# Kernel optimization log

Hardware: AMD Instinct MI355X
Metric: run time of the kernel (lower is better)

The kernel has to match this reference:

```python
import jax, jax.numpy as jnp
import numpy as np

NUM_STAB = 1e-3  # numerical_stabilizer for relu kernel


def _relu_feature(x, proj):
    # x: [B, L, H, D], proj: [M, D] -> [B, L, H, M]
    ratio = 1.0 / jnp.sqrt(jnp.asarray(proj.shape[0], x.dtype))
    return jax.nn.relu(ratio * jnp.einsum('blhd,md->blhm', x, proj)) + NUM_STAB


def setup_inputs() -> dict:
    key = jax.random.key(0)
    k1, k2, k3, k4, k5 = jax.random.split(key, 5)
    B, L, H, D, M = 16, 576, 12, 64, 8  # L = length_of_side**2 = 24**2
    return {
        'query': jax.random.normal(k1, (B, L, H, D), dtype=jnp.float32),
        'key': jax.random.normal(k2, (B, L, H, D), dtype=jnp.float32),
        'value': jax.random.normal(k3, (B, L, H, D), dtype=jnp.float32),
        'projection_matrix': jax.random.normal(k4, (M, D), dtype=jnp.float32),
        # RPE mask is nonnegative per-head mixing matrix [H, L, L]
        'mask_matrix': jax.random.uniform(k5, (H, L, L), dtype=jnp.float32),
    }


def reference(query, key, value, projection_matrix, mask_matrix):
    # ReLU kernel features (projection_matrix_type='relu')
    q_prime = _relu_feature(query, projection_matrix)  # [B, L, H, M]
    k_prime = _relu_feature(key, projection_matrix)    # [B, L, H, M]
    B, L, H, M = k_prime.shape
    D = value.shape[-1]

    # D_1[b,l,h,m,d] = k'[b,l,h,m] * v[b,l,h,d], flattened over (m,d)
    D_1 = jnp.einsum('blhm,blhd->blhmd', k_prime, value).reshape(B, L, H, M * D)
    # mask-matrix causal/RPE mixing over the L dimension (per head)
    D_1_hat = jnp.einsum('hij,bjhc->bihc', mask_matrix, D_1).reshape(B, L, H, M, D)
    D_2_hat = jnp.einsum('hij,bjhm->bihm', mask_matrix, k_prime)  # [B, L, H, M]

    av_attention = jnp.einsum('blhm,blhmd->blhd', q_prime, D_1_hat)  # [B, L, H, D]
    ks_sum = jnp.sum(D_2_hat, axis=1)                                # [B, H, M]
    normalizer = jnp.einsum('blhm,bhm->blh', q_prime, ks_sum)        # [B, L, H]
    return av_attention / normalizer[..., None]
```

## Files before the change

kernel.cpp:

```cpp
#include <hip/hip_runtime.h>
#include <hip/hip_bf16.h>


#define B_ 16
#define L_ 576
#define H_ 12
#define D_ 64
#define M_ 8
#define NUM_STAB 1e-3f
#define RATIO 0.35355339059327373f

typedef __attribute__((ext_vector_type(8))) short short8;
typedef __attribute__((ext_vector_type(4))) float f32x4;

union Pack {
    uint4 u4;
    short8 s8;
    uint2 u2[2];
    unsigned u[4];
    unsigned short us[8];
};

__device__ inline unsigned short f2bf(float x) {
    union { float f; unsigned u; } a; a.f = x;
    unsigned r = (a.u + 0x7FFFu + ((a.u >> 16) & 1u)) >> 16;
    return (unsigned short)r;
}
__device__ inline unsigned pk2(float lo, float hi) {
    __hip_bfloat162 h = __float22bfloat162_rn(make_float2(lo, hi));
    union { __hip_bfloat162 b; unsigned u; } c; c.b = h;
    return c.u;
}

#define WS_QP_OFF (H_ * L_)
#define QP_ELEMS  ((size_t)B_ * H_ * L_ * M_)

__global__ __launch_bounds__(256) void feat_kernel(const float* __restrict__ q,
                                                   const float* __restrict__ k,
                                                   const float* __restrict__ proj,
                                                   const float* __restrict__ mask,
                                                   unsigned short* __restrict__ qp,
                                                   unsigned short* __restrict__ kp,
                                                   float* __restrict__ cmask) {
    __shared__ float cred[4][16];
    const int lc = blockIdx.x, h = blockIdx.y, b = blockIdx.z, t = threadIdx.x;
    const int wv = t >> 6, l = t & 63, r8 = l >> 3, c8 = l & 7;
    const int row = lc * 32 + wv * 8 + r8;

    float4 pj0[8], pj1[8];
#pragma unroll
    for (int m = 0; m < 8; ++m) {
        pj0[m] = *(const float4*)(proj + m * 64 + c8 * 8);
        pj1[m] = *(const float4*)(proj + m * 64 + c8 * 8 + 4);
    }

#pragma unroll
    for (int s = 0; s < 2; ++s) {
        const float* src = s ? k : q;
        unsigned short* dst = s ? kp : qp;
        const float* xp = src + (((size_t)b * L_ + row) * H_ + h) * D_ + c8 * 8;
        float4 x0 = *(const float4*)xp;
        float4 x1 = *(const float4*)(xp + 4);
        x0.x *= RATIO; x0.y *= RATIO; x0.z *= RATIO; x0.w *= RATIO;
        x1.x *= RATIO; x1.y *= RATIO; x1.z *= RATIO; x1.w *= RATIO;
        float p[8];
#pragma unroll
        for (int m = 0; m < 8; ++m) {
            p[m] = x0.x * pj0[m].x + x0.y * pj0[m].y + x0.z * pj0[m].z + x0.w * pj0[m].w
                 + x1.x * pj1[m].x + x1.y * pj1[m].y + x1.z * pj1[m].z + x1.w * pj1[m].w;
        }
#pragma unroll
        for (int st = 1; st <= 4; st <<= 1) {
#pragma unroll
            for (int m = 0; m < 8; ++m) p[m] += __shfl_xor(p[m], st, 64);
        }
        float r = p[0];
        r = (c8 == 1) ? p[1] : r;
        r = (c8 == 2) ? p[2] : r;
        r = (c8 == 3) ? p[3] : r;
        r = (c8 == 4) ? p[4] : r;
        r = (c8 == 5) ? p[5] : r;
        r = (c8 == 6) ? p[6] : r;
        r = (c8 == 7) ? p[7] : r;
        r = fmaxf(r, 0.f) + NUM_STAB;
        dst[((size_t)(b * H_ + h) * L_ + row) * 8 + c8] = f2bf(r);
    }

    if (b < 2) {
        const int c = t & 15, rg = t >> 4;
        const int col0 = lc * 32 + b * 16;
        const float* mb = mask + (size_t)h * L_ * L_ + col0 + c;
        float a = 0.f;
#pragma unroll 4
        for (int k2 = 0; k2 < 36; ++k2) a += mb[(size_t)(rg + 16 * k2) * L_];
        a += __shfl_xor(a, 16, 64);
        a += __shfl_xor(a, 32, 64);
        if ((l >> 4) == 0) cred[wv][c] = a;
        __syncthreads();
        if (t < 16) cmask[h * L_ + col0 + t] = cred[0][t] + cred[1][t] + cred[2][t] + cred[3][t];
    }
}

__global__ __launch_bounds__(256, 4) void attn_kernel(const float* __restrict__ v,
                                                      const float* __restrict__ mask,
                                                      const unsigned short* __restrict__ qp,
                                                      const unsigned short* __restrict__ kp,
                                                      const float* __restrict__ cmask,
                                                      float* __restrict__ out) {
    __shared__ __align__(16) unsigned short Sp[4 * 16 * 72];
    __shared__ __align__(16) unsigned short Bt[2][64 * 72];
    __shared__ float cms[576];

    const int t = threadIdx.x;
    int id = blockIdx.x;
    const int bhi = id & 7; id >>= 3;
    const int blo = id & 1; id >>= 1;
    const int it = id % 9, h = id / 9;
    const int b = bhi * 2 + blo;
    const int i0 = it * 64;

    const int wv = t >> 6, l = t & 63, c15 = l & 15, kq = l >> 4;

    {
        const float* cmg = cmask + h * L_;
#pragma unroll
        for (int rep = 0; rep < 3; ++rep) {
            int idx = t + rep * 256;
            if (idx < 576) {
                int p = idx / 36, rem = idx - p * 36;
                int jt9 = rem >> 2, kqi = rem & 3;
                int j = jt9 * 64 + ((p >> 2) << 4) + 4 * kqi + (p & 3);
                cms[idx] = cmg[j];
            }
        }
    }

    const float* maskbase = mask + (size_t)h * L_ * L_ + (size_t)(i0 + 16 * wv + c15) * L_;
    const unsigned short* kpb = kp + (size_t)(b * H_ + h) * L_ * 8;
    const float* vb = v + ((size_t)b * L_ * H_ + h) * D_ + l;

    short8 Bq;
    {
        Pack pk; pk.u4 = make_uint4(0, 0, 0, 0);
        if (kq == 0) {
            const unsigned short* qpb = qp + ((size_t)(b * H_ + h) * L_ + i0 + 16 * wv + c15) * 8;
            pk.u4 = *(const uint4*)qpb;
        }
        Bq = pk.s8;
    }

    unsigned short* SpW = Sp + wv * 16 * 72;

    f32x4 acc0 = {0.f, 0.f, 0.f, 0.f}, acc1 = acc0, acc2 = acc0, acc3 = acc0;
    float nacc = 0.f;

    float vf[16];
    float4 mv[4];
    uint4 kraw0 = make_uint4(0, 0, 0, 0), kraw1 = kraw0;
    {
#pragma unroll
        for (int qv = 0; qv < 16; ++qv) vf[qv] = vb[(size_t)(16 * wv + qv) * (H_ * D_)];
#pragma unroll
        for (int T = 0; T < 4; ++T) mv[T] = *(const float4*)(maskbase + 16 * T + 4 * kq);
        if (kq < 2) {
            kraw0 = *(const uint4*)(kpb + (size_t)(16 * kq + c15) * 8);
            kraw1 = *(const uint4*)(kpb + (size_t)(32 + 16 * kq + c15) * 8);
        }
    }

    __syncthreads();

    for (int jt = 0; jt < 9; ++jt) {
        const int j0 = jt * 64;
        const int slab = jt & 1;

        f32x4 s[4];
        const f32x4 zz = {0.f, 0.f, 0.f, 0.f};
#pragma unroll
        for (int hh = 0; hh < 2; ++hh) {
            uint4 kr = hh ? kraw1 : kraw0;
            Pack a0, a1;
            a1.u[0] = __shfl_down(kr.x, 16, 64);
            a1.u[1] = __shfl_down(kr.y, 16, 64);
            a1.u[2] = __shfl_down(kr.z, 16, 64);
            a1.u[3] = __shfl_down(kr.w, 16, 64);
            if (kq == 0) {
                a0.u4 = kr;
            } else {
                a0.u4 = make_uint4(0, 0, 0, 0);
                a1.u4 = make_uint4(0, 0, 0, 0);
            }
            s[2 * hh]     = __builtin_amdgcn_mfma_f32_16x16x32_bf16(a0.s8, Bq, zz, 0, 0, 0);
            s[2 * hh + 1] = __builtin_amdgcn_mfma_f32_16x16x32_bf16(a1.s8, Bq, zz, 0, 0, 0);
        }

        {
            Pack p0, p1;
#pragma unroll
            for (int qv = 0; qv < 4; ++qv) p0.u[qv] = pk2(vf[2 * qv], vf[2 * qv + 1]);
#pragma unroll
            for (int qv = 0; qv < 4; ++qv) p1.u[qv] = pk2(vf[8 + 2 * qv], vf[9 + 2 * qv]);
            *(uint4*)&Bt[slab][l * 72 + 16 * wv] = p0.u4;
            *(uint4*)&Bt[slab][l * 72 + 16 * wv + 8] = p1.u4;
        }

#pragma unroll
        for (int T = 0; T < 4; ++T) {
            const float* cp = &cms[(T * 4) * 36 + jt * 4 + kq];
            float c0 = cp[0], c1 = cp[36], c2 = cp[72], c3 = cp[108];
            nacc += c0 * s[T][0] + c1 * s[T][1] + c2 * s[T][2] + c3 * s[T][3];
            float4 m4 = mv[T];
            uint2 st2;
            st2.x = pk2(s[T][0] * m4.x, s[T][1] * m4.y);
            st2.y = pk2(s[T][2] * m4.z, s[T][3] * m4.w);
            *(uint2*)&SpW[c15 * 72 + 16 * T + 4 * kq] = st2;
        }

        {
            const int jn = (jt < 8) ? j0 + 64 : 0;
#pragma unroll
            for (int qv = 0; qv < 16; ++qv) vf[qv] = vb[(size_t)(jn + 16 * wv + qv) * (H_ * D_)];
#pragma unroll
            for (int T = 0; T < 4; ++T) mv[T] = *(const float4*)(maskbase + jn + 16 * T + 4 * kq);
            if (kq < 2) {
                kraw0 = *(const uint4*)(kpb + (size_t)(jn + 16 * kq + c15) * 8);
                kraw1 = *(const uint4*)(kpb + (size_t)(jn + 32 + 16 * kq + c15) * 8);
            }
        }

        __syncthreads();

        {
            short8 As0 = *(const short8*)&SpW[c15 * 72 + kq * 8];
            short8 As1 = *(const short8*)&SpW[c15 * 72 + 32 + kq * 8];
#pragma unroll
            for (int di = 0; di < 4; ++di) {
                const unsigned short* bp = &Bt[slab][(16 * di + c15) * 72 + kq * 8];
                short8 B0 = *(const short8*)bp;
                short8 B1 = *(const short8*)(bp + 32);
                f32x4* ap = (di == 0) ? &acc0 : (di == 1) ? &acc1 : (di == 2) ? &acc2 : &acc3;
                *ap = __builtin_amdgcn_mfma_f32_16x16x32_bf16(As0, B0, *ap, 0, 0, 0);
                *ap = __builtin_amdgcn_mfma_f32_16x16x32_bf16(As1, B1, *ap, 0, 0, 0);
            }
        }
    }

    nacc += __shfl_xor(nacc, 16, 64);
    nacc += __shfl_xor(nacc, 32, 64);
    float iv[4];
#pragma unroll
    for (int r = 0; r < 4; ++r) iv[r] = 1.0f / __shfl(nacc, 4 * kq + r, 64);

    float* ob = out + (((size_t)b * L_ + i0 + 16 * wv + 4 * kq) * H_ + h) * D_ + c15;
    const f32x4 aa[4] = {acc0, acc1, acc2, acc3};
#pragma unroll
    for (int di = 0; di < 4; ++di)
#pragma unroll
        for (int r = 0; r < 4; ++r)
            ob[(size_t)r * (H_ * D_) + 16 * di] = aa[di][r] * iv[r];
}

extern "C" void kernel_launch(void* const* d_in, const int* in_sizes, int n_in,
                              void* d_out, int out_size, void* d_ws, size_t ws_size,
                              hipStream_t stream) {
    const float* q    = (const float*)d_in[0];
    const float* k    = (const float*)d_in[1];
    const float* v    = (const float*)d_in[2];
    const float* proj = (const float*)d_in[3];
    const float* mask = (const float*)d_in[4];
    float* out = (float*)d_out;

    float* ws = (float*)d_ws;
    float* cmask = ws;
    unsigned short* qp_w = (unsigned short*)(ws + WS_QP_OFF);
    unsigned short* kp_w = qp_w + QP_ELEMS;

    feat_kernel<<<dim3(L_ / 32, H_, B_), 256, 0, stream>>>(q, k, proj, mask, qp_w, kp_w, cmask);
    attn_kernel<<<1728, 256, 0, stream>>>(v, mask, qp_w, kp_w, cmask, out);
}
```

Measured before the change: 182.8 us.

## Pre-transpose V to bf16 in feature kernel and precompute normalizer weights

The feature kernel now also converts V to bf16 in a per-tile transposed layout, so the attention kernel loads it with wide vector loads instead of strided scalar float loads and per-iteration packing. The normalizer is refactored algebraically: a new small kernel computes the mask-column-sum-weighted sum of k' per (b,h), and the attention kernel computes the normalizer with a single dot product at the end instead of accumulating it every tile. The QK MFMA loading is simplified, the launch bound is raised to 5 blocks per CU, and the per-block shared column-mask staging is dropped. In exchange there is an extra kernel launch plus extra workspace traffic for the transposed V.

```diff
diff --git a/kernel.cpp b/kernel.cpp
--- a/kernel.cpp
+++ b/kernel.cpp
@@ -31,17 +31,23 @@
     union { __hip_bfloat162 b; unsigned u; } c; c.b = h;
     return c.u;
 }
-
-#define WS_QP_OFF (H_ * L_)
+__device__ inline float bf2f(unsigned short u) {
+    union { unsigned u; float f; } c; c.u = (unsigned)u << 16; return c.f;
+}
+
+#define WS_W_OFF  (H_ * L_)
+#define WS_QP_OFF (H_ * L_ + B_ * H_ * M_)
 #define QP_ELEMS  ((size_t)B_ * H_ * L_ * M_)
 
 __global__ __launch_bounds__(256) void feat_kernel(const float* __restrict__ q,
                                                    const float* __restrict__ k,
+                                                   const float* __restrict__ v,
                                                    const float* __restrict__ proj,
                                                    const float* __restrict__ mask,
                                                    unsigned short* __restrict__ qp,
                                                    unsigned short* __restrict__ kp,
-                                                   float* __restrict__ cmask) {
+                                                   float* __restrict__ cmask,
+                                                   unsigned short* __restrict__ vt) {
     __shared__ float cred[4][16];
     const int lc = blockIdx.x, h = blockIdx.y, b = blockIdx.z, t = threadIdx.x;
     const int wv = t >> 6, l = t & 63, r8 = l >> 3, c8 = l & 7;
@@ -84,6 +90,20 @@
         r = (c8 == 7) ? p[7] : r;
         r = fmaxf(r, 0.f) + NUM_STAB;
         dst[((size_t)(b * H_ + h) * L_ + row) * 8 + c8] = f2bf(r);
+    }
+
+    {
+        const int dv = t >> 2;
+        const int jl = (lc & 1) * 32 + (t & 3) * 8;
+        const int jt9 = lc >> 1;
+        const float* vsrc = v + (((size_t)b * L_ + jt9 * 64 + jl) * H_ + h) * D_ + dv;
+        float tv[8];
+#pragma unroll
+        for (int e = 0; e < 8; ++e) tv[e] = vsrc[(size_t)e * (H_ * D_)];
+        Pack pv;
+#pragma unroll
+        for (int q4 = 0; q4 < 4; ++q4) pv.u[q4] = pk2(tv[2 * q4], tv[2 * q4 + 1]);
+        *(uint4*)&vt[((size_t)(b * H_ + h) * 9 + jt9) * 4096 + dv * 64 + jl] = pv.u4;
     }
 
     if (b < 2) {
@@ -101,15 +121,44 @@
     }
 }
 
-__global__ __launch_bounds__(256, 4) void attn_kernel(const float* __restrict__ v,
-                                                      const float* __restrict__ mask,
+__global__ __launch_bounds__(64) void wsum_kernel(const unsigned short* __restrict__ kp,
+                                                  const float* __restrict__ cmask,
+                                                  float* __restrict__ wbuf) {
+    const int bh = blockIdx.x, lx = threadIdx.x;
+    const int h = bh % H_;
+    const unsigned short* kpb = kp + (size_t)bh * L_ * 8;
+    const float* cm = cmask + h * L_;
+    float a[8] = {0.f, 0.f, 0.f, 0.f, 0.f, 0.f, 0.f, 0.f};
+    for (int j = lx; j < L_; j += 64) {
+        const float c = cm[j];
+        Pack pk; pk.u4 = *(const uint4*)(kpb + (size_t)j * 8);
+#pragma unroll
+        for (int m = 0; m < 8; ++m) a[m] += c * bf2f(pk.us[m]);
+    }
+#pragma unroll
+    for (int st = 1; st < 64; st <<= 1) {
+#pragma unroll
+        for (int m = 0; m < 8; ++m) a[m] += __shfl_xor(a[m], st, 64);
+    }
+    float r = a[0];
+    r = (lx == 1) ? a[1] : r;
+    r = (lx == 2) ? a[2] : r;
+    r = (lx == 3) ? a[3] : r;
+    r = (lx == 4) ? a[4] : r;
+    r = (lx == 5) ? a[5] : r;
+    r = (lx == 6) ? a[6] : r;
+    r = (lx == 7) ? a[7] : r;
+    if (lx < 8) wbuf[(size_t)bh * 8 + lx] = r;
+}
+
+__global__ __launch_bounds__(256, 5) void attn_kernel(const float* __restrict__ mask,
                                                       const unsigned short* __restrict__ qp,
                                                       const unsigned short* __restrict__ kp,
-                                                      const float* __restrict__ cmask,
+                                                      const unsigned short* __restrict__ vt,
+                                                      const float* __restrict__ wbuf,
                                                       float* __restrict__ out) {
     __shared__ __align__(16) unsigned short Sp[4 * 16 * 72];
     __shared__ __align__(16) unsigned short Bt[2][64 * 72];
-    __shared__ float cms[576];
 
     const int t = threadIdx.x;
     int id = blockIdx.x;
@@ -120,136 +169,122 @@
     const int i0 = it * 64;
 
     const int wv = t >> 6, l = t & 63, c15 = l & 15, kq = l >> 4;
-
-    {
-        const float* cmg = cmask + h * L_;
-#pragma unroll
-        for (int rep = 0; rep < 3; ++rep) {
-            int idx = t + rep * 256;
-            if (idx < 576) {
-                int p = idx / 36, rem = idx - p * 36;
-                int jt9 = rem >> 2, kqi = rem & 3;
-                int j = jt9 * 64 + ((p >> 2) << 4) + 4 * kqi + (p & 3);
-                cms[idx] = cmg[j];
-            }
-        }
-    }
+    const int bd = t >> 3, bg = t & 7;
+    const int vt_off = bd * 64 + bg * 8;
 
     const float* maskbase = mask + (size_t)h * L_ * L_ + (size_t)(i0 + 16 * wv + c15) * L_;
     const unsigned short* kpb = kp + (size_t)(b * H_ + h) * L_ * 8;
-    const float* vb = v + ((size_t)b * L_ * H_ + h) * D_ + l;
+    const unsigned short* vtb = vt + (size_t)(b * H_ + h) * 9 * 4096;
+    unsigned short* SpW = Sp + wv * 16 * 72;
 
     short8 Bq;
     {
         Pack pk; pk.u4 = make_uint4(0, 0, 0, 0);
-        if (kq == 0) {
-            const unsigned short* qpb = qp + ((size_t)(b * H_ + h) * L_ + i0 + 16 * wv + c15) * 8;
-            pk.u4 = *(const uint4*)qpb;
-        }
+        if (kq == 0)
+            pk.u4 = *(const uint4*)(qp + ((size_t)(b * H_ + h) * L_ + i0 + 16 * wv + c15) * 8);
         Bq = pk.s8;
     }
 
-    unsigned short* SpW = Sp + wv * 16 * 72;
-
     f32x4 acc0 = {0.f, 0.f, 0.f, 0.f}, acc1 = acc0, acc2 = acc0, acc3 = acc0;
-    float nacc = 0.f;
-
-    float vf[16];
-    float4 mv[4];
-    uint4 kraw0 = make_uint4(0, 0, 0, 0), kraw1 = kraw0;
-    {
-#pragma unroll
-        for (int qv = 0; qv < 16; ++qv) vf[qv] = vb[(size_t)(16 * wv + qv) * (H_ * D_)];
-#pragma unroll
-        for (int T = 0; T < 4; ++T) mv[T] = *(const float4*)(maskbase + 16 * T + 4 * kq);
-        if (kq < 2) {
-            kraw0 = *(const uint4*)(kpb + (size_t)(16 * kq + c15) * 8);
-            kraw1 = *(const uint4*)(kpb + (size_t)(32 + 16 * kq + c15) * 8);
-        }
-    }
-
-    __syncthreads();
+    const f32x4 zz = {0.f, 0.f, 0.f, 0.f};
+
+    uint4 a0 = make_uint4(0, 0, 0, 0), a1 = a0, a2 = a0, a3 = a0;
+    uint4 vt0, vt1;
+    float4 mv0, mv1, mv2, mv3;
+    if (kq == 0) {
+        a0 = *(const uint4*)(kpb + (size_t)(c15) * 8);
+        a1 = *(const uint4*)(kpb + (size_t)(16 + c15) * 8);
+        a2 = *(const uint4*)(kpb + (size_t)(32 + c15) * 8);
+        a3 = *(const uint4*)(kpb + (size_t)(48 + c15) * 8);
+    }
+    vt0 = *(const uint4*)(vtb + vt_off);
+    vt1 = *(const uint4*)(vtb + 2048 + vt_off);
+    mv0 = *(const float4*)(maskbase + 0 + 4 * kq);
+    mv1 = *(const float4*)(maskbase + 16 + 4 * kq);
+    mv2 = *(const float4*)(maskbase + 32 + 4 * kq);
+    mv3 = *(const float4*)(maskbase + 48 + 4 * kq);
 
     for (int jt = 0; jt < 9; ++jt) {
-        const int j0 = jt * 64;
         const int slab = jt & 1;
 
-        f32x4 s[4];
-        const f32x4 zz = {0.f, 0.f, 0.f, 0.f};
-#pragma unroll
-        for (int hh = 0; hh < 2; ++hh) {
-            uint4 kr = hh ? kraw1 : kraw0;
-            Pack a0, a1;
-            a1.u[0] = __shfl_down(kr.x, 16, 64);
-            a1.u[1] = __shfl_down(kr.y, 16, 64);
-            a1.u[2] = __shfl_down(kr.z, 16, 64);
-            a1.u[3] = __shfl_down(kr.w, 16, 64);
+        f32x4 s0, s1, s2, s3;
+        {
+            Pack p0, p1, p2, p3;
+            p0.u4 = a0; p1.u4 = a1; p2.u4 = a2; p3.u4 = a3;
+            s0 = __builtin_amdgcn_mfma_f32_16x16x32_bf16(p0.s8, Bq, zz, 0, 0, 0);
+            s1 = __builtin_amdgcn_mfma_f32_16x16x32_bf16(p1.s8, Bq, zz, 0, 0, 0);
+            s2 = __builtin_amdgcn_mfma_f32_16x16x32_bf16(p2.s8, Bq, zz, 0, 0, 0);
+            s3 = __builtin_amdgcn_mfma_f32_16x16x32_bf16(p3.s8, Bq, zz, 0, 0, 0);
+        }
+
+        *(uint4*)&Bt[slab][bd * 72 + bg * 8] = vt0;
+        *(uint4*)&Bt[slab][(bd + 32) * 72 + bg * 8] = vt1;
+
+        {
+            uint2 st2;
+            st2.x = pk2(s0[0] * mv0.x, s0[1] * mv0.y);
+            st2.y = pk2(s0[2] * mv0.z, s0[3] * mv0.w);
+            *(uint2*)&SpW[c15 * 72 + 0 + 4 * kq] = st2;
+            st2.x = pk2(s1[0] * mv1.x, s1[1] * mv1.y);
+            st2.y = pk2(s1[2] * mv1.z, s1[3] * mv1.w);
+            *(uint2*)&SpW[c15 * 72 + 16 + 4 * kq] = st2;
+            st2.x = pk2(s2[0] * mv2.x, s2[1] * mv2.y);
+            st2.y = pk2(s2[2] * mv2.z, s2[3] * mv2.w);
+            *(uint2*)&SpW[c15 * 72 + 32 + 4 * kq] = st2;
+            st2.x = pk2(s3[0] * mv3.x, s3[1] * mv3.y);
+            st2.y = pk2(s3[2] * mv3.z, s3[3] * mv3.w);
+            *(uint2*)&SpW[c15 * 72 + 48 + 4 * kq] = st2;
+        }
+
+        __syncthreads();
+
+        {
+            const int jn = (jt < 8) ? jt + 1 : 0;
+            const int j0n = jn * 64;
             if (kq == 0) {
-                a0.u4 = kr;
-            } else {
-                a0.u4 = make_uint4(0, 0, 0, 0);
-                a1.u4 = make_uint4(0, 0, 0, 0);
+                a0 = *(const uint4*)(kpb + (size_t)(j0n + c15) * 8);
+                a1 = *(const uint4*)(kpb + (size_t)(j0n + 16 + c15) * 8);
+                a2 = *(const uint4*)(kpb + (size_t)(j0n + 32 + c15) * 8);
+                a3 = *(const uint4*)(kpb + (size_t)(j0n + 48 + c15) * 8);
             }
-            s[2 * hh]     = __builtin_amdgcn_mfma_f32_16x16x32_bf16(a0.s8, Bq, zz, 0, 0, 0);
-            s[2 * hh + 1] = __builtin_amdgcn_mfma_f32_16x16x32_bf16(a1.s8, Bq, zz, 0, 0, 0);
-        }
-
-        {
-            Pack p0, p1;
-#pragma unroll
-            for (int qv = 0; qv < 4; ++qv) p0.u[qv] = pk2(vf[2 * qv], vf[2 * qv + 1]);
-#pragma unroll
-            for (int qv = 0; qv < 4; ++qv) p1.u[qv] = pk2(vf[8 + 2 * qv], vf[9 + 2 * qv]);
-            *(uint4*)&Bt[slab][l * 72 + 16 * wv] = p0.u4;
-            *(uint4*)&Bt[slab][l * 72 + 16 * wv + 8] = p1.u4;
-        }
-
-#pragma unroll
-        for (int T = 0; T < 4; ++T) {
-            const float* cp = &cms[(T * 4) * 36 + jt * 4 + kq];
-            float c0 = cp[0], c1 = cp[36], c2 = cp[72], c3 = cp[108];
-            nacc += c0 * s[T][0] + c1 * s[T][1] + c2 * s[T][2] + c3 * s[T][3];
-            float4 m4 = mv[T];
-            uint2 st2;
-            st2.x = pk2(s[T][0] * m4.x, s[T][1] * m4.y);
-            st2.y = pk2(s[T][2] * m4.z, s[T][3] * m4.w);
-            *(uint2*)&SpW[c15 * 72 + 16 * T + 4 * kq] = st2;
-        }
-
-        {
-            const int jn = (jt < 8) ? j0 + 64 : 0;
-#pragma unroll
-            for (int qv = 0; qv < 16; ++qv) vf[qv] = vb[(size_t)(jn + 16 * wv + qv) * (H_ * D_)];
-#pragma unroll
-            for (int T = 0; T < 4; ++T) mv[T] = *(const float4*)(maskbase + jn + 16 * T + 4 * kq);
-            if (kq < 2) {
-                kraw0 = *(const uint4*)(kpb + (size_t)(jn + 16 * kq + c15) * 8);
-                kraw1 = *(const uint4*)(kpb + (size_t)(jn + 32 + 16 * kq + c15) * 8);
-            }
-        }
-
-        __syncthreads();
+            vt0 = *(const uint4*)(vtb + (size_t)jn * 4096 + vt_off);
+            vt1 = *(const uint4*)(vtb + (size_t)jn * 4096 + 2048 + vt_off);
+            mv0 = *(const float4*)(maskbase + j0n + 0 + 4 * kq);
+            mv1 = *(const float4*)(maskbase + j0n + 16 + 4 * kq);
+            mv2 = *(const float4*)(maskbase + j0n + 32 + 4 * kq);
+            mv3 = *(const float4*)(maskbase + j0n + 48 + 4 * kq);
+        }
 
         {
             short8 As0 = *(const short8*)&SpW[c15 * 72 + kq * 8];
             short8 As1 = *(const short8*)&SpW[c15 * 72 + 32 + kq * 8];
-#pragma unroll
-            for (int di = 0; di < 4; ++di) {
-                const unsigned short* bp = &Bt[slab][(16 * di + c15) * 72 + kq * 8];
-                short8 B0 = *(const short8*)bp;
-                short8 B1 = *(const short8*)(bp + 32);
-                f32x4* ap = (di == 0) ? &acc0 : (di == 1) ? &acc1 : (di == 2) ? &acc2 : &acc3;
-                *ap = __builtin_amdgcn_mfma_f32_16x16x32_bf16(As0, B0, *ap, 0, 0, 0);
-                *ap = __builtin_amdgcn_mfma_f32_16x16x32_bf16(As1, B1, *ap, 0, 0, 0);
-            }
-        }
-    }
-
-    nacc += __shfl_xor(nacc, 16, 64);
-    nacc += __shfl_xor(nacc, 32, 64);
+            const unsigned short* bp0 = &Bt[slab][c15 * 72 + kq * 8];
+            const unsigned short* bp1 = bp0 + 16 * 72;
+            const unsigned short* bp2 = bp0 + 32 * 72;
+            const unsigned short* bp3 = bp0 + 48 * 72;
+            acc0 = __builtin_amdgcn_mfma_f32_16x16x32_bf16(As0, *(const short8*)bp0, acc0, 0, 0, 0);
+            acc0 = __builtin_amdgcn_mfma_f32_16x16x32_bf16(As1, *(const short8*)(bp0 + 32), acc0, 0, 0, 0);
+            acc1 = __builtin_amdgcn_mfma_f32_16x16x32_bf16(As0, *(const short8*)bp1, acc1, 0, 0, 0);
+            acc1 = __builtin_amdgcn_mfma_f32_16x16x32_bf16(As1, *(const short8*)(bp1 + 32), acc1, 0, 0, 0);
+            acc2 = __builtin_amdgcn_mfma_f32_16x16x32_bf16(As0, *(const short8*)bp2, acc2, 0, 0, 0);
+            acc2 = __builtin_amdgcn_mfma_f32_16x16x32_bf16(As1, *(const short8*)(bp2 + 32), acc2, 0, 0, 0);
+            acc3 = __builtin_amdgcn_mfma_f32_16x16x32_bf16(As0, *(const short8*)bp3, acc3, 0, 0, 0);
+            acc3 = __builtin_amdgcn_mfma_f32_16x16x32_bf16(As1, *(const short8*)(bp3 + 32), acc3, 0, 0, 0);
+        }
+    }
+
+    const float* wp = wbuf + (size_t)(b * H_ + h) * 8;
+    const float4 w0 = *(const float4*)wp;
+    const float4 w1 = *(const float4*)(wp + 4);
+    Pack pq;
+    pq.u4 = *(const uint4*)(qp + ((size_t)(b * H_ + h) * L_ + i0 + 16 * wv + c15) * 8);
+    float n = bf2f(pq.us[0]) * w0.x + bf2f(pq.us[1]) * w0.y +
+              bf2f(pq.us[2]) * w0.z + bf2f(pq.us[3]) * w0.w +
+              bf2f(pq.us[4]) * w1.x + bf2f(pq.us[5]) * w1.y +
+              bf2f(pq.us[6]) * w1.z + bf2f(pq.us[7]) * w1.w;
     float iv[4];
 #pragma unroll
-    for (int r = 0; r < 4; ++r) iv[r] = 1.0f / __shfl(nacc, 4 * kq + r, 64);
+    for (int r = 0; r < 4; ++r) iv[r] = 1.0f / __shfl(n, 4 * kq + r, 64);
 
     float* ob = out + (((size_t)b * L_ + i0 + 16 * wv + 4 * kq) * H_ + h) * D_ + c15;
     const f32x4 aa[4] = {acc0, acc1, acc2, acc3};
@@ -272,9 +307,12 @@
 
     float* ws = (float*)d_ws;
     float* cmask = ws;
+    float* wbuf  = ws + WS_W_OFF;
     unsigned short* qp_w = (unsigned short*)(ws + WS_QP_OFF);
     unsigned short* kp_w = qp_w + QP_ELEMS;
-
-    feat_kernel<<<dim3(L_ / 32, H_, B_), 256, 0, stream>>>(q, k, proj, mask, qp_w, kp_w, cmask);
-    attn_kernel<<<1728, 256, 0, stream>>>(v, mask, qp_w, kp_w, cmask, out);
-}
+    unsigned short* vt_w = kp_w + QP_ELEMS;
+
+    feat_kernel<<<dim3(L_ / 32, H_, B_), 256, 0, stream>>>(q, k, v, proj, mask, qp_w, kp_w, cmask, vt_w);
+    wsum_kernel<<<B_ * H_, 64, 0, stream>>>(kp_w, cmask, wbuf);
+    attn_kernel<<<1728, 256, 0, stream>>>(mask, qp_w, kp_w, vt_w, wbuf, out);
+}
```

Measured after the change: 192.6 us. +5.4%, slower.
